# Kernel tuning notes

Measured on AMD Instinct MI355X. Metric: run time of the kernel, lower is better.

## Reference

```python
import jax, jax.numpy as jnp
import numpy as np

EPS = 1e-6
DIM = 384; HEADS = 6; POINTS = 4; LEVELS = 3; HIDDEN = 96
B = 2; H0 = 48; W0 = 48

def layernorm(x, w, b):
    m = jnp.mean(x, -1, keepdims=True)
    v = jnp.var(x, -1, keepdims=True)
    return (x - m) * jax.lax.rsqrt(v + EPS) * w + b

def make_ref_points(shapes):
    # normalized (x, y) pixel centers concatenated over levels -> [N, 2]
    pts = []
    for (Hl, Wl) in shapes:
        ry = (jnp.arange(Hl, dtype=jnp.float32) + 0.5) / Hl
        rx = (jnp.arange(Wl, dtype=jnp.float32) + 0.5) / Wl
        gy, gx = jnp.meshgrid(ry, rx, indexing='ij')
        pts.append(jnp.stack([gx.ravel(), gy.ravel()], -1))
    return jnp.concatenate(pts, 0)

def bilinear_gather(v, x, y, Hl, Wl):
    # v: [B, heads, Hl*Wl, c]; x, y: [B, heads, M] pixel coords
    # matches torch grid_sample(bilinear, align_corners=False, padding zeros)
    x0f = jnp.floor(x); y0f = jnp.floor(y)
    wx = (x - x0f)[..., None]; wy = (y - y0f)[..., None]
    x0 = x0f.astype(jnp.int32); y0 = y0f.astype(jnp.int32)
    def tap(yy, xx):
        valid = ((yy >= 0) & (yy < Hl) & (xx >= 0) & (xx < Wl)).astype(v.dtype)
        idx = jnp.clip(yy, 0, Hl - 1) * Wl + jnp.clip(xx, 0, Wl - 1)
        return jnp.take_along_axis(v, idx[..., None], axis=2) * valid[..., None]
    return (tap(y0, x0) * (1 - wx) * (1 - wy) + tap(y0, x0 + 1) * wx * (1 - wy)
            + tap(y0 + 1, x0) * (1 - wx) * wy + tap(y0 + 1, x0 + 1) * wx * wy)

def msdeform_attn(q, f, shapes, Wv, bv, Woff, boff, Watt, batt, Wout, bout):
    Bq, Nq, C = q.shape
    c = C // HEADS
    value = (f @ Wv + bv).reshape(Bq, -1, HEADS, c)
    off = (q @ Woff + boff).reshape(Bq, Nq, HEADS, LEVELS, POINTS, 2)
    att = jax.nn.softmax((q @ Watt + batt).reshape(Bq, Nq, HEADS, LEVELS * POINTS), -1)
    att = att.reshape(Bq, Nq, HEADS, LEVELS, POINTS)
    ref = make_ref_points(shapes)  # [Nq, 2]
    norm = jnp.array([[wl, hl] for (hl, wl) in shapes], dtype=q.dtype)  # [L, 2] = (W, H)
    loc = ref[None, :, None, None, None, :] + off / norm[None, None, None, :, None, :]
    starts = np.cumsum([0] + [h * w for (h, w) in shapes])
    out = jnp.zeros((Bq, Nq, HEADS, c), q.dtype)
    for l, (Hl, Wl) in enumerate(shapes):
        vl = value[:, starts[l]:starts[l + 1]].transpose(0, 2, 1, 3)  # [B,h,HW,c]
        ll = loc[:, :, :, l]  # [B,N,h,P,2]
        x = (ll[..., 0] * Wl - 0.5).transpose(0, 2, 1, 3).reshape(Bq, HEADS, Nq * POINTS)
        y = (ll[..., 1] * Hl - 0.5).transpose(0, 2, 1, 3).reshape(Bq, HEADS, Nq * POINTS)
        s = bilinear_gather(vl, x, y, Hl, Wl).reshape(Bq, HEADS, Nq, POINTS, c)
        out = out + jnp.einsum('bhnpc,bnhp->bnhc', s, att[:, :, :, l])
    return out.reshape(Bq, Nq, C) @ Wout + bout

def dwconv_levels(x, shapes, dw_w, dw_b):
    Bq, N, C = x.shape
    outs, s = [], 0
    for (Hl, Wl) in shapes:
        xi = x[:, s:s + Hl * Wl].reshape(Bq, Hl, Wl, C)
        yi = jax.lax.conv_general_dilated(xi, dw_w, (1, 1), 'SAME',
             dimension_numbers=('NHWC', 'HWIO', 'NHWC'), feature_group_count=C) + dw_b
        outs.append(yi.reshape(Bq, Hl * Wl, C))
        s += Hl * Wl
    return jnp.concatenate(outs, 1)

def setup_inputs():
    key = jax.random.key(0)
    ks = jax.random.split(key, 16)
    n = (H0 * W0) // 4
    N = 21 * n
    wfn = lambda k, s: 0.02 * jax.random.normal(k, s, jnp.float32)
    ones = lambda s: jnp.ones(s, jnp.float32)
    zeros = lambda s: jnp.zeros(s, jnp.float32)
    return {
        'query': jax.random.normal(ks[0], (B, N, DIM), jnp.float32),
        'reference_points': jax.random.uniform(ks[1], (B, N, 1, 2), dtype=jnp.float32),
        'feat': jax.random.normal(ks[2], (B, 4 * n, DIM), jnp.float32),
        'spatial_shapes': jnp.array([[2 * H0, 2 * W0], [H0, W0], [H0 // 2, W0 // 2]], jnp.int32),
        'level_start_index': jnp.array([0, 16 * n, 20 * n], jnp.int32),
        'H': H0, 'W': W0,
        'cti_qnorm_w': ones((DIM,)), 'cti_qnorm_b': zeros((DIM,)),
        'cti_fnorm_w': ones((DIM,)), 'cti_fnorm_b': zeros((DIM,)),
        'cf_qnorm_w': ones((DIM,)), 'cf_qnorm_b': zeros((DIM,)),
        'cf_fnorm_w': ones((DIM,)), 'cf_fnorm_b': zeros((DIM,)),
        'Wv': wfn(ks[3], (DIM, DIM)), 'bv': zeros((DIM,)),
        'Woff': wfn(ks[4], (DIM, HEADS * LEVELS * POINTS * 2)), 'boff': zeros((HEADS * LEVELS * POINTS * 2,)),
        'Watt': wfn(ks[5], (DIM, HEADS * LEVELS * POINTS)), 'batt': zeros((HEADS * LEVELS * POINTS,)),
        'Wout': wfn(ks[6], (DIM, DIM)), 'bout': zeros((DIM,)),
        'ffn_norm_w': ones((DIM,)), 'ffn_norm_b': zeros((DIM,)),
        'fc1_w': wfn(ks[7], (DIM, HIDDEN)), 'fc1_b': zeros((HIDDEN,)),
        'dw_w': wfn(ks[8], (3, 3, 1, HIDDEN)), 'dw_b': zeros((HIDDEN,)),
        'fc2_w': wfn(ks[9], (HIDDEN, DIM)), 'fc2_b': zeros((DIM,)),
    }

def reference(query, reference_points, feat, spatial_shapes, level_start_index, H, W,
              cti_qnorm_w, cti_qnorm_b, cti_fnorm_w, cti_fnorm_b,
              cf_qnorm_w, cf_qnorm_b, cf_fnorm_w, cf_fnorm_b,
              Wv, bv, Woff, boff, Watt, batt, Wout, bout,
              ffn_norm_w, ffn_norm_b, fc1_w, fc1_b, dw_w, dw_b, fc2_w, fc2_b):
    # NOTE: passed reference_points/spatial_shapes/level_start_index are ignored by
    # CTI_toC.forward; it recomputes them via deform_inputs_only_one(query, 16H, 16W).
    Bq, N, C = query.shape
    n = N // 21
    q = jnp.concatenate([query[:, :16 * n], query[:, 16 * n:20 * n] + feat, query[:, 20 * n:]], 1)
    shapes = [(2 * H, 2 * W), (H, W), (H // 2, W // 2)]
    qn = layernorm(q, cti_qnorm_w, cti_qnorm_b)
    fn = layernorm(q, cti_fnorm_w, cti_fnorm_b)
    aq = layernorm(qn, cf_qnorm_w, cf_qnorm_b)
    af = layernorm(fn, cf_fnorm_w, cf_fnorm_b)
    attn = msdeform_attn(aq, af, shapes, Wv, bv, Woff, boff, Watt, batt, Wout, bout)
    out = qn + attn
    h = layernorm(out, ffn_norm_w, ffn_norm_b) @ fc1_w + fc1_b
    h = dwconv_levels(h, shapes, dw_w, dw_b)
    h = jax.nn.gelu(h, approximate=False)
    h = h @ fc2_w + fc2_b
    return out + h
```

## Files before the change

### kernel.cpp

```cpp
#include <hip/hip_runtime.h>
#include <hip/hip_bf16.h>
#include <hip/hip_fp16.h>
#include <cstdint>
#include <cstddef>

#define NB 2
#define NTOK 12096
#define TOKS (NB * NTOK)
#define DIMC 384
#define NHEADS 6
#define CHD 64

typedef __attribute__((ext_vector_type(8))) __bf16 bf16x8;
typedef __attribute__((ext_vector_type(4))) float f32x4;

__device__ __forceinline__ float wave_reduce_add(float v) {
#pragma unroll
  for (int o = 32; o > 0; o >>= 1) v += __shfl_xor(v, o, 64);
  return v;
}

__device__ __forceinline__ float bf_lo(uint u) {
  union { uint i; float f; } c; c.i = u << 16; return c.f;
}
__device__ __forceinline__ float bf_hi(uint u) {
  union { uint i; float f; } c; c.i = u & 0xffff0000u; return c.f;
}
__device__ __forceinline__ ushort f2bf(float x) {
  union { __hip_bfloat16 b; ushort u; } c; c.b = __float2bfloat16(x); return c.u;
}

__device__ __forceinline__ void gload16(const ushort* g, ushort* l) {
  __builtin_amdgcn_global_load_lds(
      (const __attribute__((address_space(1))) uint*)g,
      (__attribute__((address_space(3))) uint*)l, 16, 0, 0);
}

__global__ __launch_bounds__(256) void convert_weights(
    const float* __restrict__ Wv, const float* __restrict__ Woff,
    const float* __restrict__ Watt, const float* __restrict__ Wo,
    const float* __restrict__ fc1, const float* __restrict__ fc2,
    const float* __restrict__ boff, const float* __restrict__ batt,
    const float* __restrict__ fc1b,
    __hip_bfloat16* __restrict__ Wvt, __hip_bfloat16* __restrict__ Wot,
    __hip_bfloat16* __restrict__ Wofat, __hip_bfloat16* __restrict__ fc1t,
    __hip_bfloat16* __restrict__ fc2t, float* __restrict__ bofat,
    float* __restrict__ fc1bp) {
  int id = blockIdx.x * 256 + threadIdx.x;
  if (id >= 384 * 384) return;
  int k = id % 384, n = id / 384;
  Wvt[(size_t)n * 384 + k] = __float2bfloat16(Wv[(size_t)k * 384 + n]);
  Wot[(size_t)n * 384 + k] = __float2bfloat16(Wo[(size_t)k * 384 + n]);
  if (n < 256) {
    float v = 0.f;
    if (n < 144) v = Woff[(size_t)k * 144 + n];
    else if (n < 216) v = Watt[(size_t)k * 72 + (n - 144)];
    Wofat[(size_t)n * 384 + k] = __float2bfloat16(v);
  }
  if (n < 128)
    fc1t[(size_t)n * 384 + k] = __float2bfloat16(n < 96 ? fc1[(size_t)k * 96 + n] : 0.f);
  if (k < 96)
    fc2t[(size_t)n * 96 + k] = __float2bfloat16(fc2[(size_t)k * 384 + n]);
  if (id < 256) bofat[id] = id < 144 ? boff[id] : (id < 216 ? batt[id - 144] : 0.f);
  if (id < 128) fc1bp[id] = id < 96 ? fc1b[id] : 0.f;
}

__global__ __launch_bounds__(256) void fused_ln3(
    const float* __restrict__ query, const float* __restrict__ feat,
    const float* __restrict__ w1, const float* __restrict__ b1,
    const float* __restrict__ w2, const float* __restrict__ b2,
    const float* __restrict__ w3, const float* __restrict__ b3,
    const float* __restrict__ w4, const float* __restrict__ b4,
    __hip_bfloat16* __restrict__ qn, __hip_bfloat16* __restrict__ aq,
    __hip_bfloat16* __restrict__ af) {
  int wid = (blockIdx.x * blockDim.x + threadIdx.x) >> 6;
  if (wid >= TOKS) return;
  int lane = threadIdx.x & 63;
  int bb = wid / NTOK;
  int nq = wid - bb * NTOK;

  float x[6];
  const float* qp = query + (size_t)wid * DIMC + lane;
#pragma unroll
  for (int i = 0; i < 6; ++i) x[i] = qp[64 * i];
  if (nq >= 9216 && nq < 11520) {
    const float* fp = feat + ((size_t)bb * 2304 + (nq - 9216)) * DIMC + lane;
#pragma unroll
    for (int i = 0; i < 6; ++i) x[i] += fp[64 * i];
  }

  float s = 0.f, ss = 0.f;
#pragma unroll
  for (int i = 0; i < 6; ++i) { s += x[i]; ss += x[i] * x[i]; }
  s = wave_reduce_add(s); ss = wave_reduce_add(ss);
  float mean = s * (1.f / DIMC);
  float rs = rsqrtf(ss * (1.f / DIMC) - mean * mean + 1e-6f);

  float qv[6], fv[6];
  __hip_bfloat16* qnp = qn + (size_t)wid * DIMC + lane;
#pragma unroll
  for (int i = 0; i < 6; ++i) {
    int e = lane + 64 * i;
    float xh = (x[i] - mean) * rs;
    qv[i] = xh * w1[e] + b1[e];
    fv[i] = xh * w2[e] + b2[e];
    qnp[64 * i] = __float2bfloat16(qv[i]);
  }

  s = 0.f; ss = 0.f;
#pragma unroll
  for (int i = 0; i < 6; ++i) { s += qv[i]; ss += qv[i] * qv[i]; }
  s = wave_reduce_add(s); ss = wave_reduce_add(ss);
  float m2 = s * (1.f / DIMC);
  float rs2 = rsqrtf(ss * (1.f / DIMC) - m2 * m2 + 1e-6f);
  __hip_bfloat16* aqp = aq + (size_t)wid * DIMC + lane;
#pragma unroll
  for (int i = 0; i < 6; ++i) {
    int e = lane + 64 * i;
    aqp[64 * i] = __float2bfloat16((qv[i] - m2) * rs2 * w3[e] + b3[e]);
  }

  s = 0.f; ss = 0.f;
#pragma unroll
  for (int i = 0; i < 6; ++i) { s += fv[i]; ss += fv[i] * fv[i]; }
  s = wave_reduce_add(s); ss = wave_reduce_add(ss);
  float m3 = s * (1.f / DIMC);
  float rs3 = rsqrtf(ss * (1.f / DIMC) - m3 * m3 + 1e-6f);
  __hip_bfloat16* afp = af + (size_t)wid * DIMC + lane;
#pragma unroll
  for (int i = 0; i < 6; ++i) {
    int e = lane + 64 * i;
    afp[64 * i] = __float2bfloat16((fv[i] - m3) * rs3 * w4[e] + b4[e]);
  }
}

__global__ __launch_bounds__(256) void ln_kernel(
    const float* __restrict__ x, const float* __restrict__ w,
    const float* __restrict__ b, __hip_bfloat16* __restrict__ y) {
  int wid = (blockIdx.x * blockDim.x + threadIdx.x) >> 6;
  if (wid >= TOKS) return;
  int lane = threadIdx.x & 63;
  float v[6];
  const float* xp = x + (size_t)wid * DIMC + lane;
#pragma unroll
  for (int i = 0; i < 6; ++i) v[i] = xp[64 * i];
  float s = 0.f, ss = 0.f;
#pragma unroll
  for (int i = 0; i < 6; ++i) { s += v[i]; ss += v[i] * v[i]; }
  s = wave_reduce_add(s); ss = wave_reduce_add(ss);
  float mean = s * (1.f / DIMC);
  float rs = rsqrtf(ss * (1.f / DIMC) - mean * mean + 1e-6f);
  __hip_bfloat16* yp = y + (size_t)wid * DIMC + lane;
#pragma unroll
  for (int i = 0; i < 6; ++i) {
    int e = lane + 64 * i;
    yp[64 * i] = __float2bfloat16((v[i] - mean) * rs * w[e] + b[e]);
  }
}

template <int EPI, int OUTBF16>
__global__ __launch_bounds__(256) void gemm_mfma(
    const __hip_bfloat16* __restrict__ A, const __hip_bfloat16* __restrict__ Wt,
    const float* __restrict__ bias, const void* __restrict__ Rv,
    void* __restrict__ Cv, int K, int Np, int ntx) {
  __shared__ __align__(16) ushort As[2 * 128 * 32];
  __shared__ __align__(16) ushort Bs[2 * 128 * 32];
  const int tid = threadIdx.x;

  const int nwg = gridDim.x;
  const int bid = blockIdx.x;
  const int xcd = bid & 7, off = bid >> 3;
  const int q = nwg >> 3, r = nwg & 7;
  const int tile = (xcd < r ? xcd * (q + 1) : r * (q + 1) + (xcd - r) * q) + off;
  const int tx = tile % ntx, ty = tile / ntx;
  const int m0 = ty * 128, n0 = tx * 128;

  const int lane = tid & 63, wv = tid >> 6;
  const int wm = (wv >> 1) * 64, wn = (wv & 1) * 64;
  const int rl = lane & 15, kb = lane >> 4;

  const int c0 = wv * 64 + lane;
  const int c1 = c0 + 256;
  const int r0c = c0 >> 2, b0 = (c0 & 3) ^ (r0c & 3);
  const int r1c = c1 >> 2, b1 = (c1 & 3) ^ (r1c & 3);
  const ushort* gA0 = (const ushort*)A + (size_t)(m0 + r0c) * K + b0 * 8;
  const ushort* gA1 = (const ushort*)A + (size_t)(m0 + r1c) * K + b1 * 8;
  const ushort* gB0 = (const ushort*)Wt + (size_t)(n0 + r0c) * K + b0 * 8;
  const ushort* gB1 = (const ushort*)Wt + (size_t)(n0 + r1c) * K + b1 * 8;
  ushort* lA0 = &As[(size_t)wv * 512];
  ushort* lA1 = &As[(size_t)wv * 512 + 2048];
  ushort* lB0 = &Bs[(size_t)wv * 512];
  ushort* lB1 = &Bs[(size_t)wv * 512 + 2048];

  f32x4 acc[4][4] = {};
  const int nt = K >> 5;

  gload16(gA0, lA0);
  gload16(gA1, lA1);
  gload16(gB0, lB0);
  gload16(gB1, lB1);
  __syncthreads();

  for (int t = 0; t < nt; ++t) {
    const int cb = (t & 1) << 12;
    const int nb = 4096 - cb;
    if (t + 1 < nt) {
      const int k1 = (t + 1) << 5;
      gload16(gA0 + k1, lA0 + nb);
      gload16(gA1 + k1, lA1 + nb);
      gload16(gB0 + k1, lB0 + nb);
      gload16(gB1 + k1, lB1 + nb);
    }
    bf16x8 avf[4], bvf[4];
#pragma unroll
    for (int i = 0; i < 4; ++i) {
      int ra = wm + i * 16 + rl;
      avf[i] = *(const bf16x8*)&As[cb + ra * 32 + ((kb ^ (ra & 3)) << 3)];
      int rb = wn + i * 16 + rl;
      bvf[i] = *(const bf16x8*)&Bs[cb + rb * 32 + ((kb ^ (rb & 3)) << 3)];
    }
#pragma unroll
    for (int i = 0; i < 4; ++i)
#pragma unroll
      for (int j = 0; j < 4; ++j)
        acc[i][j] = __builtin_amdgcn_mfma_f32_16x16x32_bf16(avf[i], bvf[j],
                                                            acc[i][j], 0, 0, 0);
    __syncthreads();
  }

#pragma unroll
  for (int i = 0; i < 4; ++i) {
#pragma unroll
    for (int j = 0; j < 4; ++j) {
      int col = n0 + wn + j * 16 + rl;
      float bsv = bias[col];
#pragma unroll
      for (int rr = 0; rr < 4; ++rr) {
        int row = m0 + wm + i * 16 + kb * 4 + rr;
        size_t o = (size_t)row * Np + col;
        float v = acc[i][j][rr] + bsv;
        if (EPI == 1) v += __bfloat162float(((const __hip_bfloat16*)Rv)[o]);
        if (EPI == 2) v += ((const float*)Cv)[o];
        if (OUTBF16) ((__hip_bfloat16*)Cv)[o] = __float2bfloat16(v);
        else ((float*)Cv)[o] = v;
      }
    }
  }
}

__global__ __launch_bounds__(256) void msdeform_prep(
    const float* __restrict__ offatt, uint* __restrict__ taps) {
  int id = blockIdx.x * 256 + threadIdx.x;
  if (id >= TOKS * 72) return;
  int t = id / 72, r = id - t * 72;
  int h = r / 12, lp = r - h * 12;
  int l = lp >> 2;
  int nq = t % NTOK;

  int pos, Hq, Wq;
  if (nq < 9216)       { pos = nq;         Hq = 96; Wq = 96; }
  else if (nq < 11520) { pos = nq - 9216;  Hq = 48; Wq = 48; }
  else                 { pos = nq - 11520; Hq = 24; Wq = 24; }
  int iq = pos / Wq, jq = pos - iq * Wq;
  float refx = (jq + 0.5f) / (float)Wq;
  float refy = (iq + 0.5f) / (float)Hq;

  const float* lg = offatt + (size_t)t * 256 + 144 + h * 12;
  float mx = -1e30f;
#pragma unroll
  for (int i = 0; i < 12; ++i) mx = fmaxf(mx, lg[i]);
  float sden = 0.f;
#pragma unroll
  for (int i = 0; i < 12; ++i) sden += __expf(lg[i] - mx);
  float aw = __expf(lg[lp] - mx) / sden;

  float ox = offatt[(size_t)t * 256 + h * 24 + lp * 2 + 0];
  float oy = offatt[(size_t)t * 256 + h * 24 + lp * 2 + 1];

  int Wl = 96 >> l;

  float xx = refx * (float)Wl + ox - 0.5f;
  float yy = refy * (float)Wl + oy - 0.5f;
  float x0f = floorf(xx), y0f = floorf(yy);
  int x0 = (int)x0f, y0 = (int)y0f;
  float wx = xx - x0f, wy = yy - y0f;

  bool vx0 = (x0 >= 0) & (x0 < Wl), vx1 = (x0 + 1 >= 0) & (x0 + 1 < Wl);
  bool vy0 = (y0 >= 0) & (y0 < Wl), vy1 = (y0 + 1 >= 0) & (y0 + 1 < Wl);
  int x0c = min(max(x0, 0), Wl - 1), x1c = min(max(x0 + 1, 0), Wl - 1);
  int y0c = min(max(y0, 0), Wl - 1), y1c = min(max(y0 + 1, 0), Wl - 1);

  float w00 = (vy0 && vx0) ? aw * (1.f - wx) * (1.f - wy) : 0.f;
  float w01 = (vy0 && vx1) ? aw * wx * (1.f - wy) : 0.f;
  float w10 = (vy1 && vx0) ? aw * (1.f - wx) * wy : 0.f;
  float w11 = (vy1 && vx1) ? aw * wx * wy : 0.f;

  uint i00 = (uint)(y0c * Wl + x0c), i01 = (uint)(y0c * Wl + x1c);
  uint i10 = (uint)(y1c * Wl + x0c), i11 = (uint)(y1c * Wl + x1c);

  uint4 rec;
  rec.x = ((uint)f2bf(w00) << 16) | i00;
  rec.y = ((uint)f2bf(w01) << 16) | i01;
  rec.z = ((uint)f2bf(w10) << 16) | i10;
  rec.w = ((uint)f2bf(w11) << 16) | i11;
  *(uint4*)&taps[((size_t)(t * NHEADS + h)) * 48 + lp * 4] = rec;
}

__global__ __launch_bounds__(256) void msdeform_gather(
    const __hip_bfloat16* __restrict__ value, const uint* __restrict__ taps,
    __hip_bfloat16* __restrict__ samp) {
  const int NBLK = TOKS * NHEADS / 4;
  int bid = blockIdx.x;
  int swz = (bid & 7) * (NBLK / 8) + (bid >> 3);
  int wid = __builtin_amdgcn_readfirstlane(swz * 4 + ((int)threadIdx.x >> 6));
  int lane = threadIdx.x & 63;
  int g = lane >> 3, sub = lane & 7;
  int sub16 = sub * 16;

  int t = wid / NHEADS;
  int h = wid - t * NHEADS;
  int b = t / NTOK;

  const char* vb = (const char*)value + ((size_t)(b * NTOK) * DIMC + h * CHD) * 2;
  const char* vbl[3] = {vb, vb + 9216 * DIMC * 2, vb + 11520 * DIMC * 2};

  const uint* tp = taps + (size_t)wid * 48 + g;

  float acc[8] = {0.f, 0.f, 0.f, 0.f, 0.f, 0.f, 0.f, 0.f};
#pragma unroll
  for (int i = 0; i < 6; ++i) {
    uint rec = tp[i * 8];
    float wf = bf_hi(rec);
    uint off = (rec & 0x3fffu) * (uint)(DIMC * 2) + (uint)sub16;
    uint4 d = *(const uint4*)(vbl[i >> 1] + off);
    acc[0] = fmaf(wf, bf_lo(d.x), acc[0]);
    acc[1] = fmaf(wf, bf_hi(d.x), acc[1]);
    acc[2] = fmaf(wf, bf_lo(d.y), acc[2]);
    acc[3] = fmaf(wf, bf_hi(d.y), acc[3]);
    acc[4] = fmaf(wf, bf_lo(d.z), acc[4]);
    acc[5] = fmaf(wf, bf_hi(d.z), acc[5]);
    acc[6] = fmaf(wf, bf_lo(d.w), acc[6]);
    acc[7] = fmaf(wf, bf_hi(d.w), acc[7]);
  }

#pragma unroll
  for (int r = 0; r < 8; ++r) {
    acc[r] += __shfl_xor(acc[r], 8, 64);
    acc[r] += __shfl_xor(acc[r], 16, 64);
    acc[r] += __shfl_xor(acc[r], 32, 64);
  }

  if (lane < 8) {
    uint4 o;
    o.x = ((uint)f2bf(acc[1]) << 16) | f2bf(acc[0]);
    o.y = ((uint)f2bf(acc[3]) << 16) | f2bf(acc[2]);
    o.z = ((uint)f2bf(acc[5]) << 16) | f2bf(acc[4]);
    o.w = ((uint)f2bf(acc[7]) << 16) | f2bf(acc[6]);
    *(uint4*)((char*)samp + (size_t)wid * 128 + sub16) = o;
  }
}

__global__ __launch_bounds__(256) void dwconv_gelu(
    const __hip_bfloat16* __restrict__ x, const float* __restrict__ w,
    const float* __restrict__ bias, __hip_bfloat16* __restrict__ y) {
  int id = blockIdx.x * blockDim.x + threadIdx.x;
  if (id >= TOKS * 24) return;
  int g = id % 24;
  int tn = id / 24;
  int ch0 = g * 4;
  int b = tn / NTOK, nq = tn - b * NTOK;

  int pos, Hl, Wl, st;
  if (nq < 9216)       { pos = nq;         Hl = 96; Wl = 96; st = 0; }
  else if (nq < 11520) { pos = nq - 9216;  Hl = 48; Wl = 48; st = 9216; }
  else                 { pos = nq - 11520; Hl = 24; Wl = 24; st = 11520; }
  int i = pos / Wl, j = pos - i * Wl;

  f32x4 acc = *(const f32x4*)&bias[ch0];
#pragma unroll
  for (int di = 0; di < 3; ++di) {
#pragma unroll
    for (int dj = 0; dj < 3; ++dj) {
      int ii = i + di - 1, jj = j + dj - 1;
      if (ii >= 0 && ii < Hl && jj >= 0 && jj < Wl) {
        uint2 d = *(const uint2*)&x[((size_t)(b * NTOK + st + ii * Wl + jj)) * 128 + ch0];
        f32x4 wv = *(const f32x4*)&w[(di * 3 + dj) * 96 + ch0];
        acc[0] = fmaf(bf_lo(d.x), wv[0], acc[0]);
        acc[1] = fmaf(bf_hi(d.x), wv[1], acc[1]);
        acc[2] = fmaf(bf_lo(d.y), wv[2], acc[2]);
        acc[3] = fmaf(bf_hi(d.y), wv[3], acc[3]);
      }
    }
  }
  uint2 o;
  float g0 = 0.5f * acc[0] * (1.f + erff(acc[0] * 0.70710678f));
  float g1 = 0.5f * acc[1] * (1.f + erff(acc[1] * 0.70710678f));
  float g2 = 0.5f * acc[2] * (1.f + erff(acc[2] * 0.70710678f));
  float g3 = 0.5f * acc[3] * (1.f + erff(acc[3] * 0.70710678f));
  o.x = ((uint)f2bf(g1) << 16) | f2bf(g0);
  o.y = ((uint)f2bf(g3) << 16) | f2bf(g2);
  *(uint2*)((char*)y + (size_t)tn * 192 + ch0 * 2) = o;
}

extern "C" void kernel_launch(void* const* d_in, const int* in_sizes, int n_in,
                              void* d_out, int out_size, void* d_ws, size_t ws_size,
                              hipStream_t stream) {
  const float* query = (const float*)d_in[0];
  const float* feat   = (const float*)d_in[2];
  const float* cti_qw = (const float*)d_in[7];
  const float* cti_qb = (const float*)d_in[8];
  const float* cti_fw = (const float*)d_in[9];
  const float* cti_fb = (const float*)d_in[10];
  const float* cf_qw  = (const float*)d_in[11];
  const float* cf_qb  = (const float*)d_in[12];
  const float* cf_fw  = (const float*)d_in[13];
  const float* cf_fb  = (const float*)d_in[14];
  const float* Wv     = (const float*)d_in[15];
  const float* bv     = (const float*)d_in[16];
  const float* Woff   = (const float*)d_in[17];
  const float* boff   = (const float*)d_in[18];
  const float* Watt   = (const float*)d_in[19];
  const float* batt   = (const float*)d_in[20];
  const float* Wo     = (const float*)d_in[21];
  const float* bo     = (const float*)d_in[22];
  const float* ffw    = (const float*)d_in[23];
  const float* ffb    = (const float*)d_in[24];
  const float* fc1w   = (const float*)d_in[25];
  const float* fc1b   = (const float*)d_in[26];
  const float* dww    = (const float*)d_in[27];
  const float* dwb    = (const float*)d_in[28];
  const float* fc2w   = (const float*)d_in[29];
  const float* fc2b   = (const float*)d_in[30];
  float* out = (float*)d_out;

  char* ws = (char*)d_ws;
  __hip_bfloat16* qn  = (__hip_bfloat16*)ws;
  __hip_bfloat16* aq  = (__hip_bfloat16*)(ws + 37158912);
  __hip_bfloat16* af  = (__hip_bfloat16*)(ws + 55738368);
  __hip_bfloat16* val = (__hip_bfloat16*)(ws + 74317824);
  float* offatt       = (float*)(ws + 92897280);
  char* wbase = ws + 117669888;
  __hip_bfloat16* Wvt   = (__hip_bfloat16*)(wbase + 0);
  __hip_bfloat16* Wot   = (__hip_bfloat16*)(wbase + 589824);
  __hip_bfloat16* Wofat = (__hip_bfloat16*)(wbase + 1179648);
  __hip_bfloat16* fc1t  = (__hip_bfloat16*)(wbase + 1376256);
  __hip_bfloat16* fc2t  = (__hip_bfloat16*)(wbase + 1474560);
  float* bofat          = (float*)(wbase + 1548288);
  float* fc1bp          = (float*)(wbase + 1549312);
  uint* taps = (uint*)(ws + 119220224);
  __hip_bfloat16* samp = af;
  __hip_bfloat16* lnf  = aq;
  __hip_bfloat16* h1   = (__hip_bfloat16*)offatt;
  __hip_bfloat16* h2   = (__hip_bfloat16*)(ws + 92897280 + 6193152);

  dim3 blk(256);

  convert_weights<<<576, blk, 0, stream>>>(Wv, Woff, Watt, Wo, fc1w, fc2w, boff,
                                           batt, fc1b, Wvt, Wot, Wofat, fc1t,
                                           fc2t, bofat, fc1bp);

  fused_ln3<<<TOKS / 4, blk, 0, stream>>>(query, feat, cti_qw, cti_qb, cti_fw,
                                          cti_fb, cf_qw, cf_qb, cf_fw, cf_fb,
                                          qn, aq, af);

  gemm_mfma<0, 1><<<567, blk, 0, stream>>>(af, Wvt, bv, nullptr, val, 384, 384, 3);
  gemm_mfma<0, 0><<<378, blk, 0, stream>>>(aq, Wofat, bofat, nullptr, offatt, 384, 256, 2);

  msdeform_prep<<<(TOKS * 72) / 256, blk, 0, stream>>>(offatt, taps);
  msdeform_gather<<<(TOKS * NHEADS) / 4, blk, 0, stream>>>(val, taps, samp);

  gemm_mfma<1, 0><<<567, blk, 0, stream>>>(samp, Wot, bo, qn, out, 384, 384, 3);

  ln_kernel<<<TOKS / 4, blk, 0, stream>>>(out, ffw, ffb, lnf);
  gemm_mfma<0, 1><<<189, blk, 0, stream>>>(lnf, fc1t, fc1bp, nullptr, h1, 384, 128, 1);
  dwconv_gelu<<<(TOKS * 24 + 255) / 256, blk, 0, stream>>>(h1, dww, dwb, h2);
  gemm_mfma<2, 0><<<567, blk, 0, stream>>>(h2, fc2t, fc2b, nullptr, out, 96, 384, 3);
}
```

Before: 190.5 us.

## Merge weight conversion with LN, fuse dual GEMMs, and inline tap prep into gather

Merges the weight-conversion kernel into the layernorm kernel as extra blocks. It runs the value-projection and offset/attention GEMMs as one dual-role launch, and computes the sampling taps inside the gather kernel's shared memory instead of a separate prep kernel. This removes three launches and the global round-trip of the taps buffer. In exchange, gather blocks serialize a small softmax/tap computation on 48 threads before sampling, and the merged GEMM mixes output types by branch.

```diff
diff --git a/kernel.cpp b/kernel.cpp
--- a/kernel.cpp
+++ b/kernel.cpp
@@ -36,7 +36,7 @@
       (__attribute__((address_space(3))) uint*)l, 16, 0, 0);
 }
 
-__global__ __launch_bounds__(256) void convert_weights(
+__global__ __launch_bounds__(256) void prelude_kernel(
     const float* __restrict__ Wv, const float* __restrict__ Woff,
     const float* __restrict__ Watt, const float* __restrict__ Wo,
     const float* __restrict__ fc1, const float* __restrict__ fc2,
@@ -45,27 +45,7 @@
     __hip_bfloat16* __restrict__ Wvt, __hip_bfloat16* __restrict__ Wot,
     __hip_bfloat16* __restrict__ Wofat, __hip_bfloat16* __restrict__ fc1t,
     __hip_bfloat16* __restrict__ fc2t, float* __restrict__ bofat,
-    float* __restrict__ fc1bp) {
-  int id = blockIdx.x * 256 + threadIdx.x;
-  if (id >= 384 * 384) return;
-  int k = id % 384, n = id / 384;
-  Wvt[(size_t)n * 384 + k] = __float2bfloat16(Wv[(size_t)k * 384 + n]);
-  Wot[(size_t)n * 384 + k] = __float2bfloat16(Wo[(size_t)k * 384 + n]);
-  if (n < 256) {
-    float v = 0.f;
-    if (n < 144) v = Woff[(size_t)k * 144 + n];
-    else if (n < 216) v = Watt[(size_t)k * 72 + (n - 144)];
-    Wofat[(size_t)n * 384 + k] = __float2bfloat16(v);
-  }
-  if (n < 128)
-    fc1t[(size_t)n * 384 + k] = __float2bfloat16(n < 96 ? fc1[(size_t)k * 96 + n] : 0.f);
-  if (k < 96)
-    fc2t[(size_t)n * 96 + k] = __float2bfloat16(fc2[(size_t)k * 384 + n]);
-  if (id < 256) bofat[id] = id < 144 ? boff[id] : (id < 216 ? batt[id - 144] : 0.f);
-  if (id < 128) fc1bp[id] = id < 96 ? fc1b[id] : 0.f;
-}
-
-__global__ __launch_bounds__(256) void fused_ln3(
+    float* __restrict__ fc1bp,
     const float* __restrict__ query, const float* __restrict__ feat,
     const float* __restrict__ w1, const float* __restrict__ b1,
     const float* __restrict__ w2, const float* __restrict__ b2,
@@ -73,7 +53,27 @@
     const float* __restrict__ w4, const float* __restrict__ b4,
     __hip_bfloat16* __restrict__ qn, __hip_bfloat16* __restrict__ aq,
     __hip_bfloat16* __restrict__ af) {
-  int wid = (blockIdx.x * blockDim.x + threadIdx.x) >> 6;
+  if (blockIdx.x < 576) {
+    int id = blockIdx.x * 256 + threadIdx.x;
+    int k = id % 384, n = id / 384;
+    Wvt[(size_t)n * 384 + k] = __float2bfloat16(Wv[(size_t)k * 384 + n]);
+    Wot[(size_t)n * 384 + k] = __float2bfloat16(Wo[(size_t)k * 384 + n]);
+    if (n < 256) {
+      float v = 0.f;
+      if (n < 144) v = Woff[(size_t)k * 144 + n];
+      else if (n < 216) v = Watt[(size_t)k * 72 + (n - 144)];
+      Wofat[(size_t)n * 384 + k] = __float2bfloat16(v);
+    }
+    if (n < 128)
+      fc1t[(size_t)n * 384 + k] = __float2bfloat16(n < 96 ? fc1[(size_t)k * 96 + n] : 0.f);
+    if (k < 96)
+      fc2t[(size_t)n * 96 + k] = __float2bfloat16(fc2[(size_t)k * 384 + n]);
+    if (id < 256) bofat[id] = id < 144 ? boff[id] : (id < 216 ? batt[id - 144] : 0.f);
+    if (id < 128) fc1bp[id] = id < 96 ? fc1b[id] : 0.f;
+    return;
+  }
+
+  int wid = ((blockIdx.x - 576) * blockDim.x + threadIdx.x) >> 6;
   if (wid >= TOKS) return;
   int lane = threadIdx.x & 63;
   int bb = wid / NTOK;
@@ -166,7 +166,6 @@
   __shared__ __align__(16) ushort As[2 * 128 * 32];
   __shared__ __align__(16) ushort Bs[2 * 128 * 32];
   const int tid = threadIdx.x;
-
   const int nwg = gridDim.x;
   const int bid = blockIdx.x;
   const int xcd = bid & 7, off = bid >> 3;
@@ -248,72 +247,170 @@
   }
 }
 
-__global__ __launch_bounds__(256) void msdeform_prep(
-    const float* __restrict__ offatt, uint* __restrict__ taps) {
-  int id = blockIdx.x * 256 + threadIdx.x;
-  if (id >= TOKS * 72) return;
-  int t = id / 72, r = id - t * 72;
-  int h = r / 12, lp = r - h * 12;
-  int l = lp >> 2;
-  int nq = t % NTOK;
-
-  int pos, Hq, Wq;
-  if (nq < 9216)       { pos = nq;         Hq = 96; Wq = 96; }
-  else if (nq < 11520) { pos = nq - 9216;  Hq = 48; Wq = 48; }
-  else                 { pos = nq - 11520; Hq = 24; Wq = 24; }
-  int iq = pos / Wq, jq = pos - iq * Wq;
-  float refx = (jq + 0.5f) / (float)Wq;
-  float refy = (iq + 0.5f) / (float)Hq;
-
-  const float* lg = offatt + (size_t)t * 256 + 144 + h * 12;
-  float mx = -1e30f;
-#pragma unroll
-  for (int i = 0; i < 12; ++i) mx = fmaxf(mx, lg[i]);
-  float sden = 0.f;
-#pragma unroll
-  for (int i = 0; i < 12; ++i) sden += __expf(lg[i] - mx);
-  float aw = __expf(lg[lp] - mx) / sden;
-
-  float ox = offatt[(size_t)t * 256 + h * 24 + lp * 2 + 0];
-  float oy = offatt[(size_t)t * 256 + h * 24 + lp * 2 + 1];
-
-  int Wl = 96 >> l;
-
-  float xx = refx * (float)Wl + ox - 0.5f;
-  float yy = refy * (float)Wl + oy - 0.5f;
-  float x0f = floorf(xx), y0f = floorf(yy);
-  int x0 = (int)x0f, y0 = (int)y0f;
-  float wx = xx - x0f, wy = yy - y0f;
-
-  bool vx0 = (x0 >= 0) & (x0 < Wl), vx1 = (x0 + 1 >= 0) & (x0 + 1 < Wl);
-  bool vy0 = (y0 >= 0) & (y0 < Wl), vy1 = (y0 + 1 >= 0) & (y0 + 1 < Wl);
-  int x0c = min(max(x0, 0), Wl - 1), x1c = min(max(x0 + 1, 0), Wl - 1);
-  int y0c = min(max(y0, 0), Wl - 1), y1c = min(max(y0 + 1, 0), Wl - 1);
-
-  float w00 = (vy0 && vx0) ? aw * (1.f - wx) * (1.f - wy) : 0.f;
-  float w01 = (vy0 && vx1) ? aw * wx * (1.f - wy) : 0.f;
-  float w10 = (vy1 && vx0) ? aw * (1.f - wx) * wy : 0.f;
-  float w11 = (vy1 && vx1) ? aw * wx * wy : 0.f;
-
-  uint i00 = (uint)(y0c * Wl + x0c), i01 = (uint)(y0c * Wl + x1c);
-  uint i10 = (uint)(y1c * Wl + x0c), i11 = (uint)(y1c * Wl + x1c);
-
-  uint4 rec;
-  rec.x = ((uint)f2bf(w00) << 16) | i00;
-  rec.y = ((uint)f2bf(w01) << 16) | i01;
-  rec.z = ((uint)f2bf(w10) << 16) | i10;
-  rec.w = ((uint)f2bf(w11) << 16) | i11;
-  *(uint4*)&taps[((size_t)(t * NHEADS + h)) * 48 + lp * 4] = rec;
+__global__ __launch_bounds__(256) void gemm_dual(
+    const __hip_bfloat16* __restrict__ A1, const __hip_bfloat16* __restrict__ W1,
+    const float* __restrict__ bias1, void* __restrict__ C1,
+    const __hip_bfloat16* __restrict__ A2, const __hip_bfloat16* __restrict__ W2,
+    const float* __restrict__ bias2, void* __restrict__ C2) {
+  __shared__ __align__(16) ushort As[2 * 128 * 32];
+  __shared__ __align__(16) ushort Bs[2 * 128 * 32];
+  const int tid = threadIdx.x;
+  const int gbid = blockIdx.x;
+  const bool r2 = gbid >= 567;
+  const __hip_bfloat16* A = r2 ? A2 : A1;
+  const __hip_bfloat16* Wt = r2 ? W2 : W1;
+  const float* bias = r2 ? bias2 : bias1;
+  void* Cv = r2 ? C2 : C1;
+  const int Np = r2 ? 256 : 384, ntx = r2 ? 2 : 3;
+  const int lbid = r2 ? gbid - 567 : gbid;
+  const int lnwg = r2 ? 378 : 567;
+  const int K = 384;
+
+  const int xcd = lbid & 7, off = lbid >> 3;
+  const int q = lnwg >> 3, r = lnwg & 7;
+  const int tile = (xcd < r ? xcd * (q + 1) : r * (q + 1) + (xcd - r) * q) + off;
+  const int tx = tile % ntx, ty = tile / ntx;
+  const int m0 = ty * 128, n0 = tx * 128;
+
+  const int lane = tid & 63, wv = tid >> 6;
+  const int wm = (wv >> 1) * 64, wn = (wv & 1) * 64;
+  const int rl = lane & 15, kb = lane >> 4;
+
+  const int c0 = wv * 64 + lane;
+  const int c1 = c0 + 256;
+  const int r0c = c0 >> 2, b0 = (c0 & 3) ^ (r0c & 3);
+  const int r1c = c1 >> 2, b1 = (c1 & 3) ^ (r1c & 3);
+  const ushort* gA0 = (const ushort*)A + (size_t)(m0 + r0c) * K + b0 * 8;
+  const ushort* gA1 = (const ushort*)A + (size_t)(m0 + r1c) * K + b1 * 8;
+  const ushort* gB0 = (const ushort*)Wt + (size_t)(n0 + r0c) * K + b0 * 8;
+  const ushort* gB1 = (const ushort*)Wt + (size_t)(n0 + r1c) * K + b1 * 8;
+  ushort* lA0 = &As[(size_t)wv * 512];
+  ushort* lA1 = &As[(size_t)wv * 512 + 2048];
+  ushort* lB0 = &Bs[(size_t)wv * 512];
+  ushort* lB1 = &Bs[(size_t)wv * 512 + 2048];
+
+  f32x4 acc[4][4] = {};
+  const int nt = K >> 5;
+
+  gload16(gA0, lA0);
+  gload16(gA1, lA1);
+  gload16(gB0, lB0);
+  gload16(gB1, lB1);
+  __syncthreads();
+
+  for (int t = 0; t < nt; ++t) {
+    const int cb = (t & 1) << 12;
+    const int nb = 4096 - cb;
+    if (t + 1 < nt) {
+      const int k1 = (t + 1) << 5;
+      gload16(gA0 + k1, lA0 + nb);
+      gload16(gA1 + k1, lA1 + nb);
+      gload16(gB0 + k1, lB0 + nb);
+      gload16(gB1 + k1, lB1 + nb);
+    }
+    bf16x8 avf[4], bvf[4];
+#pragma unroll
+    for (int i = 0; i < 4; ++i) {
+      int ra = wm + i * 16 + rl;
+      avf[i] = *(const bf16x8*)&As[cb + ra * 32 + ((kb ^ (ra & 3)) << 3)];
+      int rb = wn + i * 16 + rl;
+      bvf[i] = *(const bf16x8*)&Bs[cb + rb * 32 + ((kb ^ (rb & 3)) << 3)];
+    }
+#pragma unroll
+    for (int i = 0; i < 4; ++i)
+#pragma unroll
+      for (int j = 0; j < 4; ++j)
+        acc[i][j] = __builtin_amdgcn_mfma_f32_16x16x32_bf16(avf[i], bvf[j],
+                                                            acc[i][j], 0, 0, 0);
+    __syncthreads();
+  }
+
+#pragma unroll
+  for (int i = 0; i < 4; ++i) {
+#pragma unroll
+    for (int j = 0; j < 4; ++j) {
+      int col = n0 + wn + j * 16 + rl;
+      float bsv = bias[col];
+#pragma unroll
+      for (int rr = 0; rr < 4; ++rr) {
+        int row = m0 + wm + i * 16 + kb * 4 + rr;
+        size_t o = (size_t)row * Np + col;
+        float v = acc[i][j][rr] + bsv;
+        if (!r2) ((__hip_bfloat16*)Cv)[o] = __float2bfloat16(v);
+        else ((float*)Cv)[o] = v;
+      }
+    }
+  }
 }
 
 __global__ __launch_bounds__(256) void msdeform_gather(
-    const __hip_bfloat16* __restrict__ value, const uint* __restrict__ taps,
+    const __hip_bfloat16* __restrict__ value, const float* __restrict__ offatt,
     __hip_bfloat16* __restrict__ samp) {
   const int NBLK = TOKS * NHEADS / 4;
   int bid = blockIdx.x;
   int swz = (bid & 7) * (NBLK / 8) + (bid >> 3);
-  int wid = __builtin_amdgcn_readfirstlane(swz * 4 + ((int)threadIdx.x >> 6));
-  int lane = threadIdx.x & 63;
+  int wid0 = swz * 4;
+  int tid = threadIdx.x;
+
+  __shared__ __align__(16) uint srec[192];
+
+  if (tid < 48) {
+    int pair = tid / 12, lp = tid - pair * 12;
+    int wid = wid0 + pair;
+    int t = wid / NHEADS, h = wid - t * NHEADS;
+    int l = lp >> 2;
+    int nq = t % NTOK;
+
+    int pos, Hq, Wq;
+    if (nq < 9216)       { pos = nq;         Hq = 96; Wq = 96; }
+    else if (nq < 11520) { pos = nq - 9216;  Hq = 48; Wq = 48; }
+    else                 { pos = nq - 11520; Hq = 24; Wq = 24; }
+    int iq = pos / Wq, jq = pos - iq * Wq;
+    float refx = (jq + 0.5f) / (float)Wq;
+    float refy = (iq + 0.5f) / (float)Hq;
+
+    const float* lg = offatt + (size_t)t * 256 + 144 + h * 12;
+    float mx = -1e30f;
+#pragma unroll
+    for (int i = 0; i < 12; ++i) mx = fmaxf(mx, lg[i]);
+    float sden = 0.f;
+#pragma unroll
+    for (int i = 0; i < 12; ++i) sden += __expf(lg[i] - mx);
+    float aw = __expf(lg[lp] - mx) / sden;
+
+    float ox = offatt[(size_t)t * 256 + h * 24 + lp * 2 + 0];
+    float oy = offatt[(size_t)t * 256 + h * 24 + lp * 2 + 1];
+
+    int Wl = 96 >> l;
+
+    float xx = refx * (float)Wl + ox - 0.5f;
+    float yy = refy * (float)Wl + oy - 0.5f;
+    float x0f = floorf(xx), y0f = floorf(yy);
+    int x0 = (int)x0f, y0 = (int)y0f;
+    float wx = xx - x0f, wy = yy - y0f;
+
+    bool vx0 = (x0 >= 0) & (x0 < Wl), vx1 = (x0 + 1 >= 0) & (x0 + 1 < Wl);
+    bool vy0 = (y0 >= 0) & (y0 < Wl), vy1 = (y0 + 1 >= 0) & (y0 + 1 < Wl);
+    int x0c = min(max(x0, 0), Wl - 1), x1c = min(max(x0 + 1, 0), Wl - 1);
+    int y0c = min(max(y0, 0), Wl - 1), y1c = min(max(y0 + 1, 0), Wl - 1);
+
+    float w00 = (vy0 && vx0) ? aw * (1.f - wx) * (1.f - wy) : 0.f;
+    float w01 = (vy0 && vx1) ? aw * wx * (1.f - wy) : 0.f;
+    float w10 = (vy1 && vx0) ? aw * (1.f - wx) * wy : 0.f;
+    float w11 = (vy1 && vx1) ? aw * wx * wy : 0.f;
+
+    uint4 rec;
+    rec.x = ((uint)f2bf(w00) << 16) | (uint)(y0c * Wl + x0c);
+    rec.y = ((uint)f2bf(w01) << 16) | (uint)(y0c * Wl + x1c);
+    rec.z = ((uint)f2bf(w10) << 16) | (uint)(y1c * Wl + x0c);
+    rec.w = ((uint)f2bf(w11) << 16) | (uint)(y1c * Wl + x1c);
+    *(uint4*)&srec[pair * 48 + lp * 4] = rec;
+  }
+  __syncthreads();
+
+  int w = tid >> 6;
+  int wid = __builtin_amdgcn_readfirstlane(wid0 + w);
+  int lane = tid & 63;
   int g = lane >> 3, sub = lane & 7;
   int sub16 = sub * 16;
 
@@ -324,7 +421,7 @@
   const char* vb = (const char*)value + ((size_t)(b * NTOK) * DIMC + h * CHD) * 2;
   const char* vbl[3] = {vb, vb + 9216 * DIMC * 2, vb + 11520 * DIMC * 2};
 
-  const uint* tp = taps + (size_t)wid * 48 + g;
+  const uint* tp = &srec[w * 48 + g];
 
   float acc[8] = {0.f, 0.f, 0.f, 0.f, 0.f, 0.f, 0.f, 0.f};
 #pragma unroll
@@ -447,7 +544,6 @@
   __hip_bfloat16* fc2t  = (__hip_bfloat16*)(wbase + 1474560);
   float* bofat          = (float*)(wbase + 1548288);
   float* fc1bp          = (float*)(wbase + 1549312);
-  uint* taps = (uint*)(ws + 119220224);
   __hip_bfloat16* samp = af;
   __hip_bfloat16* lnf  = aq;
   __hip_bfloat16* h1   = (__hip_bfloat16*)offatt;
@@ -455,19 +551,14 @@
 
   dim3 blk(256);
 
-  convert_weights<<<576, blk, 0, stream>>>(Wv, Woff, Watt, Wo, fc1w, fc2w, boff,
-                                           batt, fc1b, Wvt, Wot, Wofat, fc1t,
-                                           fc2t, bofat, fc1bp);
-
-  fused_ln3<<<TOKS / 4, blk, 0, stream>>>(query, feat, cti_qw, cti_qb, cti_fw,
-                                          cti_fb, cf_qw, cf_qb, cf_fw, cf_fb,
-                                          qn, aq, af);
-
-  gemm_mfma<0, 1><<<567, blk, 0, stream>>>(af, Wvt, bv, nullptr, val, 384, 384, 3);
-  gemm_mfma<0, 0><<<378, blk, 0, stream>>>(aq, Wofat, bofat, nullptr, offatt, 384, 256, 2);
-
-  msdeform_prep<<<(TOKS * 72) / 256, blk, 0, stream>>>(offatt, taps);
-  msdeform_gather<<<(TOKS * NHEADS) / 4, blk, 0, stream>>>(val, taps, samp);
+  prelude_kernel<<<576 + TOKS / 4, blk, 0, stream>>>(
+      Wv, Woff, Watt, Wo, fc1w, fc2w, boff, batt, fc1b, Wvt, Wot, Wofat, fc1t,
+      fc2t, bofat, fc1bp, query, feat, cti_qw, cti_qb, cti_fw, cti_fb, cf_qw,
+      cf_qb, cf_fw, cf_fb, qn, aq, af);
+
+  gemm_dual<<<945, blk, 0, stream>>>(af, Wvt, bv, val, aq, Wofat, bofat, offatt);
+
+  msdeform_gather<<<(TOKS * NHEADS) / 4, blk, 0, stream>>>(val, offatt, samp);
 
   gemm_mfma<1, 0><<<567, blk, 0, stream>>>(samp, Wot, bo, qn, out, 384, 384, 3);
 
```

Result: faster. 186.0 us (-2.3%).
